# Kernel tuning notes

Hardware: AMD Instinct MI355X
Metric: run time of the kernel (lower is better)

Reference implementation:

```python
import jax, jax.numpy as jnp
import numpy as np
from jax import lax

B, T_IN, D = 32, 512, 384
F = 384      # x_predictor_filter_size
K = 3        # kernel, padding=1 -> same length
LN_EPS = 1e-5


def setup_inputs() -> dict:
    key = jax.random.key(0)
    ks = jax.random.split(key, 8)
    s = 0.02
    return {
        "x": jax.random.normal(ks[0], (B, T_IN, D), dtype=jnp.float32),
        "target": jax.random.randint(ks[1], (B, T_IN), 0, 8, dtype=jnp.int32),
        "mel_max_length": 4096,
        "conv1_w": jax.random.normal(ks[2], (F, D, K), dtype=jnp.float32) * s,
        "conv1_b": jnp.zeros((F,), jnp.float32),
        "ln1_g": jnp.ones((F,), jnp.float32),
        "ln1_b": jnp.zeros((F,), jnp.float32),
        "conv2_w": jax.random.normal(ks[3], (F, F, K), dtype=jnp.float32) * s,
        "conv2_b": jnp.zeros((F,), jnp.float32),
        "ln2_g": jnp.ones((F,), jnp.float32),
        "ln2_b": jnp.zeros((F,), jnp.float32),
        "lin_w": jax.random.normal(ks[4], (F, 1), dtype=jnp.float32) * s,
        "lin_b": jnp.zeros((1,), jnp.float32),
    }


def _conv1d_same(h_ncl, w, b):
    # h_ncl: [B, C_in, T], w: [C_out, C_in, K], padding=1
    out = lax.conv_general_dilated(h_ncl, w, window_strides=(1,), padding=[(1, 1)],
                                   dimension_numbers=("NCH", "OIH", "NCH"))
    return out + b[None, :, None]


def _layernorm(h, g, b):
    mu = jnp.mean(h, axis=-1, keepdims=True)
    var = jnp.var(h, axis=-1, keepdims=True)
    return (h - mu) * lax.rsqrt(var + LN_EPS) * g + b


def _duration_predictor(x, conv1_w, conv1_b, ln1_g, ln1_b, conv2_w, conv2_b, ln2_g, ln2_b, lin_w, lin_b):
    h = _conv1d_same(jnp.transpose(x, (0, 2, 1)), conv1_w, conv1_b)       # [B,F,T]
    h = jax.nn.relu(_layernorm(jnp.transpose(h, (0, 2, 1)), ln1_g, ln1_b))  # [B,T,F]
    h = _conv1d_same(jnp.transpose(h, (0, 2, 1)), conv2_w, conv2_b)
    h = jax.nn.relu(_layernorm(jnp.transpose(h, (0, 2, 1)), ln2_g, ln2_b))
    return (h @ lin_w + lin_b)[..., 0]  # [B, T_in]


def _length_regulate(x, target, mel_max_length):
    # Equivalent to alignment @ x with one-hot alignment built by create_alignment,
    # expressed as a duration-indexed gather (same math, no dense [B,Tout,Tin]).
    ends = jnp.cumsum(target, axis=1)                 # [B, T_in]
    m = jnp.arange(mel_max_length)                    # [T_out]
    idx = jax.vmap(lambda e: jnp.searchsorted(e, m, side="right"))(ends)  # [B, T_out]
    valid = idx < target.shape[1]                     # frames past total duration -> zero pad
    idx = jnp.minimum(idx, target.shape[1] - 1)
    out = jnp.take_along_axis(x, idx[:, :, None], axis=1)  # [B, T_out, D]
    return out * valid[:, :, None].astype(x.dtype)


def reference(x, target, mel_max_length, conv1_w, conv1_b, ln1_g, ln1_b,
              conv2_w, conv2_b, ln2_g, ln2_b, lin_w, lin_b):
    dur_pred = _duration_predictor(x, conv1_w, conv1_b, ln1_g, ln1_b,
                                   conv2_w, conv2_b, ln2_g, ln2_b, lin_w, lin_b)
    output = _length_regulate(x, target, mel_max_length)
    return output, dur_pred
```

## Files before the change

### kernel.cpp

```cpp
#include <hip/hip_runtime.h>
#include <cstdint>
#include <cstddef>

#define B_   32
#define TIN  512
#define D_   384
#define F_   384
#define TOUT 4096

typedef __bf16 bf16x8 __attribute__((ext_vector_type(8)));
typedef float  f32x4  __attribute__((ext_vector_type(4)));
typedef unsigned short u16x8 __attribute__((ext_vector_type(8)));

__device__ __forceinline__ unsigned short f2bf(float f) {
  unsigned int u = __float_as_uint(f);
  u += 0x7fff + ((u >> 16) & 1);
  return (unsigned short)(u >> 16);
}

__device__ __forceinline__ void load16_to_lds(const void* g, void* l) {
  __builtin_amdgcn_global_load_lds(
      (const __attribute__((address_space(1))) unsigned int*)g,
      (__attribute__((address_space(3))) unsigned int*)l, 16, 0, 0);
}

#define GB 2048

__global__ __launch_bounds__(256) void gather_prep(
    const float* __restrict__ w1, const float* __restrict__ w2,
    unsigned short* __restrict__ Wt1, unsigned short* __restrict__ Wt2,
    const int* __restrict__ target,
    const f32x4* __restrict__ x4, f32x4* __restrict__ out4) {
  int bx = blockIdx.x;
  int tid = threadIdx.x;

  if (bx < GB) {
    __shared__ int ends[512];
    __shared__ int ps[256];
    __shared__ int idx_s[64];
    int b  = bx >> 6;
    int r0 = (bx & 63) * 64;
    int a0 = target[b * TIN + 2 * tid];
    int a1 = target[b * TIN + 2 * tid + 1];
    ps[tid] = a0 + a1;
    __syncthreads();
    for (int off = 1; off < 256; off <<= 1) {
      int add = (tid >= off) ? ps[tid - off] : 0;
      __syncthreads();
      ps[tid] += add;
      __syncthreads();
    }
    int incl = ps[tid];
    ends[2 * tid + 1] = incl;
    ends[2 * tid]     = incl - a1;
    __syncthreads();
    if (tid < 64) {
      int m = r0 + tid;
      int lo = 0, hi = 512;
      while (lo < hi) {
        int mid = (lo + hi) >> 1;
        if (ends[mid] <= m) lo = mid + 1; else hi = mid;
      }
      idx_s[tid] = (lo < TIN) ? lo : -1;
    }
    __syncthreads();
    const f32x4* xb = x4 + (size_t)b * (TIN * 96);
    f32x4* ob = out4 + ((size_t)b * TOUT + r0) * 96;
    #pragma unroll 4
    for (int it = 0; it < 24; ++it) {
      int j = it * 256 + tid;
      int row = j / 96;
      int c = j - row * 96;
      int id = idx_s[row];
      f32x4 v = {0.f, 0.f, 0.f, 0.f};
      if (id >= 0) v = xb[id * 96 + c];
      __builtin_nontemporal_store(v, ob + j);
    }
    return;
  }
  bx -= GB;

  {
    int g = bx * 256 + tid;
    const int FD = F_ * D_;
    int which = g >= FD;
    const float* w = which ? w2 : w1;
    unsigned short* o = which ? Wt2 : Wt1;
    int e = g - which * FD;
    o[e]          = f2bf(w[e * 3 + 0]);
    o[FD + e]     = f2bf(w[e * 3 + 1]);
    o[2 * FD + e] = f2bf(w[e * 3 + 2]);
  }
}

__global__ __launch_bounds__(512, 1) void conv(
    const unsigned short* __restrict__ Wt1, const unsigned short* __restrict__ Wt2,
    const float* __restrict__ b1, const float* __restrict__ g1, const float* __restrict__ be1,
    const float* __restrict__ b2, const float* __restrict__ g2, const float* __restrict__ be2,
    const float* __restrict__ lw, const float* __restrict__ lb,
    float* __restrict__ dur, const float4* __restrict__ x4) {
  __shared__ __attribute__((aligned(16))) char smem[112128];
  char* As = smem;
  char* Bs = smem + 62976;

  const int tid = threadIdx.x;
  const int cb  = blockIdx.x;

  const int wave = tid >> 6;
  const int lane = tid & 63;
  const int quad = lane >> 4;
  const int l15  = lane & 15;
  const int wn   = wave * 48;
  const int m0   = cb * 64;
  const int b    = m0 >> 9;
  const int t0   = m0 & 511;
  const int arow = tid >> 2;
  const int acol = (tid & 3) * 8;

  for (int p = 0; p < 7; ++p) {
    int ch = p * 512 + tid;
    if (ch < 3264) {
      int row = ch / 48;
      int ci  = ch - row * 48;
      int t   = t0 - 2 + row;
      u16x8 val;
      if ((unsigned)t >= (unsigned)TIN) {
        val = (u16x8)0;
      } else {
        const float4* xr = (const float4*)x4 + ((size_t)(b * TIN + t)) * 96 + ci * 2;
        float4 v0 = xr[0], v1 = xr[1];
        val[0] = f2bf(v0.x); val[1] = f2bf(v0.y); val[2] = f2bf(v0.z); val[3] = f2bf(v0.w);
        val[4] = f2bf(v1.x); val[5] = f2bf(v1.y); val[6] = f2bf(v1.z); val[7] = f2bf(v1.w);
      }
      unsigned int byte = ((unsigned int)(row * 768 + ci * 16)) ^ (((unsigned)row & 7u) << 4);
      *(u16x8*)(As + byte) = val;
    }
  }

  auto stageB = [&](const unsigned short* __restrict__ Wt, int kc, int buf) {
    int kw = kc / 12;
    int d0 = (kc - kw * 12) * 32;
    const unsigned short* src = Wt + (size_t)(kw * F_ + arow) * D_ + d0 + acol;
    char* dst = Bs + buf * 24576 + wave * 1024;
    for (int r = 0; r < 3; ++r)
      load16_to_lds(src + (size_t)(r * 128) * D_, dst + r * 8192);
  };

  f32x4 acc1[5][3];
  for (int i = 0; i < 5; ++i)
    for (int j = 0; j < 3; ++j)
      acc1[i][j] = (f32x4){0.f, 0.f, 0.f, 0.f};

  stageB(Wt1, 0, 0);
  __syncthreads();
  int cur = 0;
  #pragma unroll 1
  for (int kc = 0; kc < 36; ++kc) {
    if (kc < 35) stageB(Wt1, kc + 1, cur ^ 1);
    int kw = kc / 12;
    int d0 = (kc - kw * 12) * 32;
    const char* Bc = Bs + cur * 24576;
    bf16x8 bv[3];
    for (int ni = 0; ni < 3; ++ni)
      bv[ni] = *(const bf16x8*)(Bc + (wn + ni * 16 + l15) * 64 + quad * 16);
    int rb = l15 + kw;
    unsigned int sw = (((unsigned)rb) & 7u) << 4;
    unsigned int base = (unsigned int)(rb * 768 + d0 * 2 + quad * 16);
    bf16x8 av[5];
    for (int mi = 0; mi < 5; ++mi)
      av[mi] = *(const bf16x8*)(As + ((base + mi * 12288) ^ sw));
    for (int mi = 0; mi < 5; ++mi)
      for (int ni = 0; ni < 3; ++ni)
        acc1[mi][ni] = __builtin_amdgcn_mfma_f32_16x16x32_bf16(av[mi], bv[ni], acc1[mi][ni], 0, 0, 0);
    __syncthreads();
    cur ^= 1;
  }

  {
    float gv[6], bev[6];
    for (int j = 0; j < 6; ++j) {
      int c = lane + j * 64;
      gv[j] = g1[c]; bev[j] = be1[c];
    }
    float bb[3];
    for (int ni = 0; ni < 3; ++ni) bb[ni] = b1[wn + ni * 16 + l15];
    char* scr = Bs;

    for (int mi = 0; mi < 5; ++mi) {
      __syncthreads();
      for (int ni = 0; ni < 3; ++ni) {
        int cc = wn + ni * 16 + l15;
        for (int r = 0; r < 4; ++r) {
          int wr = quad * 4 + r;
          unsigned int byte = ((unsigned int)(wr * 1536 + cc * 4)) ^ ((((unsigned)wr >> 2) & 3u) << 4);
          *(float*)(scr + byte) = acc1[mi][ni][r] + bb[ni];
        }
      }
      __syncthreads();
      for (int rr = 0; rr < 2; ++rr) {
        int lr = wave * 2 + rr;
        int h = mi * 16 + lr;
        if (h >= 66) continue;
        unsigned int swr = ((((unsigned)lr) >> 2) & 3u) << 4;
        float v[6], s = 0.f, ss = 0.f;
        for (int j = 0; j < 6; ++j) {
          unsigned int byte = ((unsigned int)(lr * 1536 + (lane + j * 64) * 4)) ^ swr;
          v[j] = *(const float*)(scr + byte);
          s += v[j]; ss += v[j] * v[j];
        }
        for (int off = 32; off; off >>= 1) {
          s  += __shfl_xor(s, off);
          ss += __shfl_xor(ss, off);
        }
        float mean = s * (1.f / 384.f);
        float var  = ss * (1.f / 384.f) - mean * mean;
        float rstd = rsqrtf(var + 1e-5f);
        int th = t0 - 1 + h;
        bool valid = (unsigned)th < (unsigned)TIN;
        unsigned int hb = (((unsigned)h) & 7u) << 4;
        for (int j = 0; j < 6; ++j) {
          float y = (v[j] - mean) * rstd * gv[j] + bev[j];
          y = y > 0.f ? y : 0.f;
          if (!valid) y = 0.f;
          unsigned int byte = ((unsigned int)(h * 768 + (lane + j * 64) * 2)) ^ hb;
          *(unsigned short*)(As + byte) = f2bf(y);
        }
      }
    }
  }

  __syncthreads();
  f32x4 acc2[4][3];
  for (int i = 0; i < 4; ++i)
    for (int j = 0; j < 3; ++j)
      acc2[i][j] = (f32x4){0.f, 0.f, 0.f, 0.f};

  stageB(Wt2, 0, 0);
  __syncthreads();
  cur = 0;
  #pragma unroll 1
  for (int kc = 0; kc < 36; ++kc) {
    if (kc < 35) stageB(Wt2, kc + 1, cur ^ 1);
    int kw = kc / 12;
    int d0 = (kc - kw * 12) * 32;
    const char* Bc = Bs + cur * 24576;
    bf16x8 bv[3];
    for (int ni = 0; ni < 3; ++ni)
      bv[ni] = *(const bf16x8*)(Bc + (wn + ni * 16 + l15) * 64 + quad * 16);
    int rb = l15 + kw;
    unsigned int sw = (((unsigned)rb) & 7u) << 4;
    unsigned int base = (unsigned int)(rb * 768 + d0 * 2 + quad * 16);
    bf16x8 av[4];
    for (int mi = 0; mi < 4; ++mi)
      av[mi] = *(const bf16x8*)(As + ((base + mi * 12288) ^ sw));
    for (int mi = 0; mi < 4; ++mi)
      for (int ni = 0; ni < 3; ++ni)
        acc2[mi][ni] = __builtin_amdgcn_mfma_f32_16x16x32_bf16(av[mi], bv[ni], acc2[mi][ni], 0, 0, 0);
    __syncthreads();
    cur ^= 1;
  }

  {
    float gv[6], bev[6], lwv[6];
    for (int j = 0; j < 6; ++j) {
      int c = lane + j * 64;
      gv[j] = g2[c]; bev[j] = be2[c]; lwv[j] = lw[c];
    }
    float bb[3];
    for (int ni = 0; ni < 3; ++ni) bb[ni] = b2[wn + ni * 16 + l15];
    float lbv = lb[0];
    char* scr = Bs;

    for (int mi = 0; mi < 4; ++mi) {
      __syncthreads();
      for (int ni = 0; ni < 3; ++ni) {
        int cc = wn + ni * 16 + l15;
        for (int r = 0; r < 4; ++r) {
          int wr = quad * 4 + r;
          unsigned int byte = ((unsigned int)(wr * 1536 + cc * 4)) ^ ((((unsigned)wr >> 2) & 3u) << 4);
          *(float*)(scr + byte) = acc2[mi][ni][r] + bb[ni];
        }
      }
      __syncthreads();
      for (int rr = 0; rr < 2; ++rr) {
        int lr = wave * 2 + rr;
        int m = mi * 16 + lr;
        unsigned int swr = ((((unsigned)lr) >> 2) & 3u) << 4;
        float v[6], s = 0.f, ss = 0.f;
        for (int j = 0; j < 6; ++j) {
          unsigned int byte = ((unsigned int)(lr * 1536 + (lane + j * 64) * 4)) ^ swr;
          v[j] = *(const float*)(scr + byte);
          s += v[j]; ss += v[j] * v[j];
        }
        for (int off = 32; off; off >>= 1) {
          s  += __shfl_xor(s, off);
          ss += __shfl_xor(ss, off);
        }
        float mean = s * (1.f / 384.f);
        float var  = ss * (1.f / 384.f) - mean * mean;
        float rstd = rsqrtf(var + 1e-5f);
        float a = 0.f;
        for (int j = 0; j < 6; ++j) {
          float y = (v[j] - mean) * rstd * gv[j] + bev[j];
          y = y > 0.f ? y : 0.f;
          a += y * lwv[j];
        }
        for (int off = 32; off; off >>= 1) a += __shfl_xor(a, off);
        if (lane == 0) dur[m0 + m] = a + lbv;
      }
    }
  }
}

extern "C" void kernel_launch(void* const* d_in, const int* in_sizes, int n_in,
                              void* d_out, int out_size, void* d_ws, size_t ws_size,
                              hipStream_t stream) {
  const float* x      = (const float*)d_in[0];
  const int*   target = (const int*)d_in[1];
  const float* w1  = (const float*)d_in[3];
  const float* b1  = (const float*)d_in[4];
  const float* g1  = (const float*)d_in[5];
  const float* be1 = (const float*)d_in[6];
  const float* w2  = (const float*)d_in[7];
  const float* b2  = (const float*)d_in[8];
  const float* g2  = (const float*)d_in[9];
  const float* be2 = (const float*)d_in[10];
  const float* lw  = (const float*)d_in[11];
  const float* lb  = (const float*)d_in[12];

  float* out = (float*)d_out;
  float* dur = out + (size_t)B_ * TOUT * D_;

  char* ws = (char*)d_ws;
  unsigned short* Wt1  = (unsigned short*)(ws);
  unsigned short* Wt2  = (unsigned short*)(ws + 884736);

  gather_prep<<<dim3(GB + 1152), dim3(256), 0, stream>>>(
      w1, w2, Wt1, Wt2, target, (const f32x4*)x, (f32x4*)out);
  conv<<<dim3(256), dim3(512), 0, stream>>>(
      Wt1, Wt2, b1, g1, be1, b2, g2, be2, lw, lb, dur, (const float4*)x);
}
```

Before: 331.1 us.

## Fuse gather into conv kernel, load weights directly to registers, reduce LN via stats

Moves the length-regulator gather into the same launch as the conv blocks, so the memory-bound gather overlaps with the MFMA-heavy convolution; weight conversion becomes its own small kernel. The conv loops now read B weights straight from global memory into registers with a one-step prefetch instead of double-buffered LDS staging, which cuts LDS use and removes the per-iteration barrier, allowing more blocks per CU. LayerNorm is computed from the accumulators in place using per-wave partial sums reduced through a small LDS stats table, replacing the scratch write and re-read. The risks are global-load latency on the weights without LDS sharing across waves, and scheduling interaction between the conv and gather blocks.

```diff
diff --git a/kernel.cpp b/kernel.cpp
--- a/kernel.cpp
+++ b/kernel.cpp
@@ -18,43 +18,50 @@
   return (unsigned short)(u >> 16);
 }
 
-__device__ __forceinline__ void load16_to_lds(const void* g, void* l) {
-  __builtin_amdgcn_global_load_lds(
-      (const __attribute__((address_space(1))) unsigned int*)g,
-      (__attribute__((address_space(3))) unsigned int*)l, 16, 0, 0);
+__global__ __launch_bounds__(256) void prep_w(
+    const float* __restrict__ w1, const float* __restrict__ w2,
+    unsigned short* __restrict__ Wt1, unsigned short* __restrict__ Wt2) {
+  int g = blockIdx.x * 256 + threadIdx.x;
+  const int FD = F_ * D_;
+  int which = g >= FD;
+  const float* w = which ? w2 : w1;
+  unsigned short* o = which ? Wt2 : Wt1;
+  int e = g - which * FD;
+  o[e]          = f2bf(w[e * 3 + 0]);
+  o[FD + e]     = f2bf(w[e * 3 + 1]);
+  o[2 * FD + e] = f2bf(w[e * 3 + 2]);
 }
 
-#define GB 2048
-
-__global__ __launch_bounds__(256) void gather_prep(
-    const float* __restrict__ w1, const float* __restrict__ w2,
-    unsigned short* __restrict__ Wt1, unsigned short* __restrict__ Wt2,
-    const int* __restrict__ target,
+#define NCONV 256
+#define NGATH 1024
+
+__global__ __launch_bounds__(512, 4) void fused(
+    const unsigned short* __restrict__ Wt1, const unsigned short* __restrict__ Wt2,
+    const float* __restrict__ b1, const float* __restrict__ g1, const float* __restrict__ be1,
+    const float* __restrict__ b2, const float* __restrict__ g2, const float* __restrict__ be2,
+    const float* __restrict__ lw, const float* __restrict__ lb,
+    float* __restrict__ dur, const int* __restrict__ target,
     const f32x4* __restrict__ x4, f32x4* __restrict__ out4) {
-  int bx = blockIdx.x;
-  int tid = threadIdx.x;
-
-  if (bx < GB) {
-    __shared__ int ends[512];
-    __shared__ int ps[256];
-    __shared__ int idx_s[64];
-    int b  = bx >> 6;
-    int r0 = (bx & 63) * 64;
-    int a0 = target[b * TIN + 2 * tid];
-    int a1 = target[b * TIN + 2 * tid + 1];
-    ps[tid] = a0 + a1;
-    __syncthreads();
-    for (int off = 1; off < 256; off <<= 1) {
-      int add = (tid >= off) ? ps[tid - off] : 0;
+  __shared__ __attribute__((aligned(16))) char smem[68736];
+
+  const int tid = threadIdx.x;
+  const int bx  = blockIdx.x;
+
+  if (bx >= NCONV) {
+    int gi = bx - NCONV;
+    int* ends  = (int*)smem;
+    int* idx_s = (int*)(smem + 2048);
+    int b  = gi >> 5;
+    int r0 = (gi & 31) * 128;
+    ends[tid] = target[b * TIN + tid];
+    __syncthreads();
+    for (int off = 1; off < 512; off <<= 1) {
+      int add = (tid >= off) ? ends[tid - off] : 0;
       __syncthreads();
-      ps[tid] += add;
+      ends[tid] += add;
       __syncthreads();
     }
-    int incl = ps[tid];
-    ends[2 * tid + 1] = incl;
-    ends[2 * tid]     = incl - a1;
-    __syncthreads();
-    if (tid < 64) {
+    if (tid < 128) {
       int m = r0 + tid;
       int lo = 0, hi = 512;
       while (lo < hi) {
@@ -68,7 +75,7 @@
     f32x4* ob = out4 + ((size_t)b * TOUT + r0) * 96;
     #pragma unroll 4
     for (int it = 0; it < 24; ++it) {
-      int j = it * 256 + tid;
+      int j = it * 512 + tid;
       int row = j / 96;
       int c = j - row * 96;
       int id = idx_s[row];
@@ -78,44 +85,19 @@
     }
     return;
   }
-  bx -= GB;
-
-  {
-    int g = bx * 256 + tid;
-    const int FD = F_ * D_;
-    int which = g >= FD;
-    const float* w = which ? w2 : w1;
-    unsigned short* o = which ? Wt2 : Wt1;
-    int e = g - which * FD;
-    o[e]          = f2bf(w[e * 3 + 0]);
-    o[FD + e]     = f2bf(w[e * 3 + 1]);
-    o[2 * FD + e] = f2bf(w[e * 3 + 2]);
-  }
-}
-
-__global__ __launch_bounds__(512, 1) void conv(
-    const unsigned short* __restrict__ Wt1, const unsigned short* __restrict__ Wt2,
-    const float* __restrict__ b1, const float* __restrict__ g1, const float* __restrict__ be1,
-    const float* __restrict__ b2, const float* __restrict__ g2, const float* __restrict__ be2,
-    const float* __restrict__ lw, const float* __restrict__ lb,
-    float* __restrict__ dur, const float4* __restrict__ x4) {
-  __shared__ __attribute__((aligned(16))) char smem[112128];
+
   char* As = smem;
-  char* Bs = smem + 62976;
-
-  const int tid = threadIdx.x;
-  const int cb  = blockIdx.x;
+  float* stats  = (float*)(smem + 62976);
+  float* stats2 = (float*)(smem + 68096);
 
   const int wave = tid >> 6;
   const int lane = tid & 63;
   const int quad = lane >> 4;
   const int l15  = lane & 15;
   const int wn   = wave * 48;
-  const int m0   = cb * 64;
+  const int m0   = bx * 64;
   const int b    = m0 >> 9;
   const int t0   = m0 & 511;
-  const int arow = tid >> 2;
-  const int acol = (tid & 3) * 8;
 
   for (int p = 0; p < 7; ++p) {
     int ch = p * 512 + tid;
@@ -127,187 +109,197 @@
       if ((unsigned)t >= (unsigned)TIN) {
         val = (u16x8)0;
       } else {
-        const float4* xr = (const float4*)x4 + ((size_t)(b * TIN + t)) * 96 + ci * 2;
-        float4 v0 = xr[0], v1 = xr[1];
-        val[0] = f2bf(v0.x); val[1] = f2bf(v0.y); val[2] = f2bf(v0.z); val[3] = f2bf(v0.w);
-        val[4] = f2bf(v1.x); val[5] = f2bf(v1.y); val[6] = f2bf(v1.z); val[7] = f2bf(v1.w);
+        const f32x4* xr = x4 + ((size_t)(b * TIN + t)) * 96 + ci * 2;
+        f32x4 v0 = xr[0], v1 = xr[1];
+        val[0] = f2bf(v0[0]); val[1] = f2bf(v0[1]); val[2] = f2bf(v0[2]); val[3] = f2bf(v0[3]);
+        val[4] = f2bf(v1[0]); val[5] = f2bf(v1[1]); val[6] = f2bf(v1[2]); val[7] = f2bf(v1[3]);
       }
       unsigned int byte = ((unsigned int)(row * 768 + ci * 16)) ^ (((unsigned)row & 7u) << 4);
       *(u16x8*)(As + byte) = val;
     }
   }
-
-  auto stageB = [&](const unsigned short* __restrict__ Wt, int kc, int buf) {
-    int kw = kc / 12;
-    int d0 = (kc - kw * 12) * 32;
-    const unsigned short* src = Wt + (size_t)(kw * F_ + arow) * D_ + d0 + acol;
-    char* dst = Bs + buf * 24576 + wave * 1024;
-    for (int r = 0; r < 3; ++r)
-      load16_to_lds(src + (size_t)(r * 128) * D_, dst + r * 8192);
-  };
-
-  f32x4 acc1[5][3];
+  __syncthreads();
+
+  f32x4 acc[5][3];
   for (int i = 0; i < 5; ++i)
     for (int j = 0; j < 3; ++j)
-      acc1[i][j] = (f32x4){0.f, 0.f, 0.f, 0.f};
-
-  stageB(Wt1, 0, 0);
-  __syncthreads();
-  int cur = 0;
-  #pragma unroll 1
-  for (int kc = 0; kc < 36; ++kc) {
-    if (kc < 35) stageB(Wt1, kc + 1, cur ^ 1);
-    int kw = kc / 12;
-    int d0 = (kc - kw * 12) * 32;
-    const char* Bc = Bs + cur * 24576;
-    bf16x8 bv[3];
+      acc[i][j] = (f32x4){0.f, 0.f, 0.f, 0.f};
+
+  {
+    const unsigned short* Bb = Wt1 + (size_t)(wn + l15) * D_ + quad * 8;
+    bf16x8 bvn[3];
     for (int ni = 0; ni < 3; ++ni)
-      bv[ni] = *(const bf16x8*)(Bc + (wn + ni * 16 + l15) * 64 + quad * 16);
-    int rb = l15 + kw;
-    unsigned int sw = (((unsigned)rb) & 7u) << 4;
-    unsigned int base = (unsigned int)(rb * 768 + d0 * 2 + quad * 16);
-    bf16x8 av[5];
+      bvn[ni] = *(const bf16x8*)(Bb + ni * (16 * D_));
+    #pragma unroll 1
+    for (int kc = 0; kc < 36; ++kc) {
+      bf16x8 bv[3];
+      bv[0] = bvn[0]; bv[1] = bvn[1]; bv[2] = bvn[2];
+      if (kc < 35) {
+        int kn = kc + 1;
+        int kw2 = kn / 12, d02 = (kn - kw2 * 12) * 32;
+        const unsigned short* Bk = Bb + (size_t)kw2 * (F_ * D_) + d02;
+        for (int ni = 0; ni < 3; ++ni)
+          bvn[ni] = *(const bf16x8*)(Bk + ni * (16 * D_));
+      }
+      int kw = kc / 12, d0 = (kc - kw * 12) * 32;
+      int rb = l15 + kw;
+      unsigned int sw = (((unsigned)rb) & 7u) << 4;
+      unsigned int base = (unsigned int)(rb * 768 + d0 * 2 + quad * 16);
+      bf16x8 av[5];
+      for (int mi = 0; mi < 5; ++mi)
+        av[mi] = *(const bf16x8*)(As + ((base + mi * 12288) ^ sw));
+      for (int mi = 0; mi < 5; ++mi)
+        for (int ni = 0; ni < 3; ++ni)
+          acc[mi][ni] = __builtin_amdgcn_mfma_f32_16x16x32_bf16(av[mi], bv[ni], acc[mi][ni], 0, 0, 0);
+    }
+  }
+
+  {
+    float g1v[3], be1v[3], bb1[3];
+    for (int ni = 0; ni < 3; ++ni) {
+      int c = wn + ni * 16 + l15;
+      g1v[ni] = g1[c]; be1v[ni] = be1[c]; bb1[ni] = b1[c];
+    }
     for (int mi = 0; mi < 5; ++mi)
-      av[mi] = *(const bf16x8*)(As + ((base + mi * 12288) ^ sw));
+      for (int r = 0; r < 4; ++r) {
+        float s = 0.f, ssq = 0.f;
+        for (int ni = 0; ni < 3; ++ni) {
+          float y = acc[mi][ni][r] + bb1[ni];
+          s += y; ssq += y * y;
+        }
+        for (int off = 1; off < 16; off <<= 1) {
+          s   += __shfl_xor(s, off);
+          ssq += __shfl_xor(ssq, off);
+        }
+        if (l15 == 0) {
+          int row = mi * 16 + quad * 4 + r;
+          stats[(row * 8 + wave) * 2 + 0] = s;
+          stats[(row * 8 + wave) * 2 + 1] = ssq;
+        }
+      }
+    __syncthreads();
+    if (tid < 80) {
+      float s = 0.f, ssq = 0.f;
+      for (int w = 0; w < 8; ++w) {
+        s   += stats[(tid * 8 + w) * 2 + 0];
+        ssq += stats[(tid * 8 + w) * 2 + 1];
+      }
+      float mean = s * (1.f / 384.f);
+      float var  = ssq * (1.f / 384.f) - mean * mean;
+      stats2[tid * 2 + 0] = mean;
+      stats2[tid * 2 + 1] = rsqrtf(var + 1e-5f);
+    }
+    __syncthreads();
     for (int mi = 0; mi < 5; ++mi)
-      for (int ni = 0; ni < 3; ++ni)
-        acc1[mi][ni] = __builtin_amdgcn_mfma_f32_16x16x32_bf16(av[mi], bv[ni], acc1[mi][ni], 0, 0, 0);
-    __syncthreads();
-    cur ^= 1;
-  }
-
-  {
-    float gv[6], bev[6];
-    for (int j = 0; j < 6; ++j) {
-      int c = lane + j * 64;
-      gv[j] = g1[c]; bev[j] = be1[c];
-    }
-    float bb[3];
-    for (int ni = 0; ni < 3; ++ni) bb[ni] = b1[wn + ni * 16 + l15];
-    char* scr = Bs;
-
-    for (int mi = 0; mi < 5; ++mi) {
-      __syncthreads();
-      for (int ni = 0; ni < 3; ++ni) {
-        int cc = wn + ni * 16 + l15;
-        for (int r = 0; r < 4; ++r) {
-          int wr = quad * 4 + r;
-          unsigned int byte = ((unsigned int)(wr * 1536 + cc * 4)) ^ ((((unsigned)wr >> 2) & 3u) << 4);
-          *(float*)(scr + byte) = acc1[mi][ni][r] + bb[ni];
-        }
-      }
-      __syncthreads();
-      for (int rr = 0; rr < 2; ++rr) {
-        int lr = wave * 2 + rr;
-        int h = mi * 16 + lr;
-        if (h >= 66) continue;
-        unsigned int swr = ((((unsigned)lr) >> 2) & 3u) << 4;
-        float v[6], s = 0.f, ss = 0.f;
-        for (int j = 0; j < 6; ++j) {
-          unsigned int byte = ((unsigned int)(lr * 1536 + (lane + j * 64) * 4)) ^ swr;
-          v[j] = *(const float*)(scr + byte);
-          s += v[j]; ss += v[j] * v[j];
-        }
-        for (int off = 32; off; off >>= 1) {
-          s  += __shfl_xor(s, off);
-          ss += __shfl_xor(ss, off);
-        }
-        float mean = s * (1.f / 384.f);
-        float var  = ss * (1.f / 384.f) - mean * mean;
-        float rstd = rsqrtf(var + 1e-5f);
-        int th = t0 - 1 + h;
-        bool valid = (unsigned)th < (unsigned)TIN;
-        unsigned int hb = (((unsigned)h) & 7u) << 4;
-        for (int j = 0; j < 6; ++j) {
-          float y = (v[j] - mean) * rstd * gv[j] + bev[j];
-          y = y > 0.f ? y : 0.f;
-          if (!valid) y = 0.f;
-          unsigned int byte = ((unsigned int)(h * 768 + (lane + j * 64) * 2)) ^ hb;
-          *(unsigned short*)(As + byte) = f2bf(y);
-        }
-      }
-    }
-  }
-
-  __syncthreads();
+      for (int r = 0; r < 4; ++r) {
+        int row = mi * 16 + quad * 4 + r;
+        if (row < 66) {
+          float mean = stats2[row * 2 + 0];
+          float rstd = stats2[row * 2 + 1];
+          int th = t0 - 1 + row;
+          bool valid = (unsigned)th < (unsigned)TIN;
+          unsigned int hb = (((unsigned)row) & 7u) << 4;
+          for (int ni = 0; ni < 3; ++ni) {
+            float y = (acc[mi][ni][r] + bb1[ni] - mean) * rstd * g1v[ni] + be1v[ni];
+            y = y > 0.f ? y : 0.f;
+            if (!valid) y = 0.f;
+            unsigned int byte = ((unsigned int)(row * 768 + (wn + ni * 16 + l15) * 2)) ^ hb;
+            *(unsigned short*)(As + byte) = f2bf(y);
+          }
+        }
+      }
+    __syncthreads();
+  }
+
   f32x4 acc2[4][3];
   for (int i = 0; i < 4; ++i)
     for (int j = 0; j < 3; ++j)
       acc2[i][j] = (f32x4){0.f, 0.f, 0.f, 0.f};
 
-  stageB(Wt2, 0, 0);
-  __syncthreads();
-  cur = 0;
-  #pragma unroll 1
-  for (int kc = 0; kc < 36; ++kc) {
-    if (kc < 35) stageB(Wt2, kc + 1, cur ^ 1);
-    int kw = kc / 12;
-    int d0 = (kc - kw * 12) * 32;
-    const char* Bc = Bs + cur * 24576;
-    bf16x8 bv[3];
+  {
+    const unsigned short* Bb = Wt2 + (size_t)(wn + l15) * D_ + quad * 8;
+    bf16x8 bvn[3];
     for (int ni = 0; ni < 3; ++ni)
-      bv[ni] = *(const bf16x8*)(Bc + (wn + ni * 16 + l15) * 64 + quad * 16);
-    int rb = l15 + kw;
-    unsigned int sw = (((unsigned)rb) & 7u) << 4;
-    unsigned int base = (unsigned int)(rb * 768 + d0 * 2 + quad * 16);
-    bf16x8 av[4];
+      bvn[ni] = *(const bf16x8*)(Bb + ni * (16 * D_));
+    #pragma unroll 1
+    for (int kc = 0; kc < 36; ++kc) {
+      bf16x8 bv[3];
+      bv[0] = bvn[0]; bv[1] = bvn[1]; bv[2] = bvn[2];
+      if (kc < 35) {
+        int kn = kc + 1;
+        int kw2 = kn / 12, d02 = (kn - kw2 * 12) * 32;
+        const unsigned short* Bk = Bb + (size_t)kw2 * (F_ * D_) + d02;
+        for (int ni = 0; ni < 3; ++ni)
+          bvn[ni] = *(const bf16x8*)(Bk + ni * (16 * D_));
+      }
+      int kw = kc / 12, d0 = (kc - kw * 12) * 32;
+      int rb = l15 + kw;
+      unsigned int sw = (((unsigned)rb) & 7u) << 4;
+      unsigned int base = (unsigned int)(rb * 768 + d0 * 2 + quad * 16);
+      bf16x8 av[4];
+      for (int mi = 0; mi < 4; ++mi)
+        av[mi] = *(const bf16x8*)(As + ((base + mi * 12288) ^ sw));
+      for (int mi = 0; mi < 4; ++mi)
+        for (int ni = 0; ni < 3; ++ni)
+          acc2[mi][ni] = __builtin_amdgcn_mfma_f32_16x16x32_bf16(av[mi], bv[ni], acc2[mi][ni], 0, 0, 0);
+    }
+  }
+
+  {
+    float g2v[3], be2v[3], lwv[3], bb2[3];
+    for (int ni = 0; ni < 3; ++ni) {
+      int c = wn + ni * 16 + l15;
+      g2v[ni] = g2[c]; be2v[ni] = be2[c]; lwv[ni] = lw[c]; bb2[ni] = b2[c];
+    }
     for (int mi = 0; mi < 4; ++mi)
-      av[mi] = *(const bf16x8*)(As + ((base + mi * 12288) ^ sw));
+      for (int r = 0; r < 4; ++r) {
+        float s = 0.f, ssq = 0.f;
+        for (int ni = 0; ni < 3; ++ni) {
+          float y = acc2[mi][ni][r] + bb2[ni];
+          s += y; ssq += y * y;
+        }
+        for (int off = 1; off < 16; off <<= 1) {
+          s   += __shfl_xor(s, off);
+          ssq += __shfl_xor(ssq, off);
+        }
+        if (l15 == 0) {
+          int row = mi * 16 + quad * 4 + r;
+          stats[(row * 8 + wave) * 2 + 0] = s;
+          stats[(row * 8 + wave) * 2 + 1] = ssq;
+        }
+      }
+    __syncthreads();
+    if (tid < 64) {
+      float s = 0.f, ssq = 0.f;
+      for (int w = 0; w < 8; ++w) {
+        s   += stats[(tid * 8 + w) * 2 + 0];
+        ssq += stats[(tid * 8 + w) * 2 + 1];
+      }
+      float mean = s * (1.f / 384.f);
+      float var  = ssq * (1.f / 384.f) - mean * mean;
+      stats2[tid * 2 + 0] = mean;
+      stats2[tid * 2 + 1] = rsqrtf(var + 1e-5f);
+    }
+    __syncthreads();
     for (int mi = 0; mi < 4; ++mi)
-      for (int ni = 0; ni < 3; ++ni)
-        acc2[mi][ni] = __builtin_amdgcn_mfma_f32_16x16x32_bf16(av[mi], bv[ni], acc2[mi][ni], 0, 0, 0);
-    __syncthreads();
-    cur ^= 1;
-  }
-
-  {
-    float gv[6], bev[6], lwv[6];
-    for (int j = 0; j < 6; ++j) {
-      int c = lane + j * 64;
-      gv[j] = g2[c]; bev[j] = be2[c]; lwv[j] = lw[c];
-    }
-    float bb[3];
-    for (int ni = 0; ni < 3; ++ni) bb[ni] = b2[wn + ni * 16 + l15];
-    float lbv = lb[0];
-    char* scr = Bs;
-
-    for (int mi = 0; mi < 4; ++mi) {
-      __syncthreads();
-      for (int ni = 0; ni < 3; ++ni) {
-        int cc = wn + ni * 16 + l15;
-        for (int r = 0; r < 4; ++r) {
-          int wr = quad * 4 + r;
-          unsigned int byte = ((unsigned int)(wr * 1536 + cc * 4)) ^ ((((unsigned)wr >> 2) & 3u) << 4);
-          *(float*)(scr + byte) = acc2[mi][ni][r] + bb[ni];
-        }
-      }
-      __syncthreads();
-      for (int rr = 0; rr < 2; ++rr) {
-        int lr = wave * 2 + rr;
-        int m = mi * 16 + lr;
-        unsigned int swr = ((((unsigned)lr) >> 2) & 3u) << 4;
-        float v[6], s = 0.f, ss = 0.f;
-        for (int j = 0; j < 6; ++j) {
-          unsigned int byte = ((unsigned int)(lr * 1536 + (lane + j * 64) * 4)) ^ swr;
-          v[j] = *(const float*)(scr + byte);
-          s += v[j]; ss += v[j] * v[j];
-        }
-        for (int off = 32; off; off >>= 1) {
-          s  += __shfl_xor(s, off);
-          ss += __shfl_xor(ss, off);
-        }
-        float mean = s * (1.f / 384.f);
-        float var  = ss * (1.f / 384.f) - mean * mean;
-        float rstd = rsqrtf(var + 1e-5f);
+      for (int r = 0; r < 4; ++r) {
+        int row = mi * 16 + quad * 4 + r;
+        float mean = stats2[row * 2 + 0];
+        float rstd = stats2[row * 2 + 1];
         float a = 0.f;
-        for (int j = 0; j < 6; ++j) {
-          float y = (v[j] - mean) * rstd * gv[j] + bev[j];
+        for (int ni = 0; ni < 3; ++ni) {
+          float y = (acc2[mi][ni][r] + bb2[ni] - mean) * rstd * g2v[ni] + be2v[ni];
           y = y > 0.f ? y : 0.f;
-          a += y * lwv[j];
-        }
-        for (int off = 32; off; off >>= 1) a += __shfl_xor(a, off);
-        if (lane == 0) dur[m0 + m] = a + lbv;
-      }
+          a += y * lwv[ni];
+        }
+        for (int off = 1; off < 16; off <<= 1) a += __shfl_xor(a, off);
+        if (l15 == 0) stats[(row * 8 + wave) * 2 + 0] = a;
+      }
+    __syncthreads();
+    if (tid < 64) {
+      float a = 0.f;
+      for (int w = 0; w < 8; ++w) a += stats[(tid * 8 + w) * 2 + 0];
+      dur[m0 + tid] = a + lb[0];
     }
   }
 }
@@ -332,11 +324,11 @@
   float* dur = out + (size_t)B_ * TOUT * D_;
 
   char* ws = (char*)d_ws;
-  unsigned short* Wt1  = (unsigned short*)(ws);
-  unsigned short* Wt2  = (unsigned short*)(ws + 884736);
-
-  gather_prep<<<dim3(GB + 1152), dim3(256), 0, stream>>>(
-      w1, w2, Wt1, Wt2, target, (const f32x4*)x, (f32x4*)out);
-  conv<<<dim3(256), dim3(512), 0, stream>>>(
-      Wt1, Wt2, b1, g1, be1, b2, g2, be2, lw, lb, dur, (const float4*)x);
+  unsigned short* Wt1 = (unsigned short*)(ws);
+  unsigned short* Wt2 = (unsigned short*)(ws + 884736);
+
+  prep_w<<<dim3(1152), dim3(256), 0, stream>>>(w1, w2, Wt1, Wt2);
+  fused<<<dim3(NCONV + NGATH), dim3(512), 0, stream>>>(
+      Wt1, Wt2, b1, g1, be1, b2, g2, be2, lw, lb,
+      dur, target, (const f32x4*)x, (f32x4*)out);
 }
```

New measurement: 283.5 us. 1.17x faster.
